# Optimization experiments

Hardware: AMD Instinct MI355X
Metric: run time of the kernel (lower is better)

The kernel has to match this reference:

```python
import jax, jax.numpy as jnp
import numpy as np

EPS = 1e-8


def _dtw_distance(cost):
    """Classic DTW DP: D[i,j] = cost[i,j] + min(D[i-1,j], D[i-1,j-1], D[i,j-1]).
    Rows are processed with lax.scan; the within-row left-to-right recurrence
    D[j] = min(a[j], D[j-1] + c[j]) is solved in closed form as a min-plus scan:
    with S = cumsum(c), D = cummin(a - S) + S.
    """
    # first row: only horizontal moves -> running cumsum
    d0 = jnp.cumsum(cost[0])

    def row_step(prev, c):
        # prev: D[i-1, :]  (shape [m]);  c: cost[i, :]
        prev_diag = jnp.concatenate([jnp.full((1,), jnp.inf, prev.dtype), prev[:-1]])
        a = c + jnp.minimum(prev, prev_diag)          # candidate from above / diagonal
        S = jnp.cumsum(c)
        d = jax.lax.cummin(a - S) + S                 # folds in the left-neighbor path
        return d, None

    d_last, _ = jax.lax.scan(row_step, d0, cost[1:])
    return d_last[-1]


def setup_inputs() -> dict:
    key = jax.random.key(0)
    k1, k2 = jax.random.split(key)
    N1, N2, D = 4096, 4096, 1024
    return {
        "trajectory1": jax.random.normal(k1, (N1, D), dtype=jnp.float32),
        "trajectory2": jax.random.normal(k2, (N2, D), dtype=jnp.float32),
    }


def reference(trajectory1, trajectory2):
    # cosine distance matrix: 1 - <t1_hat, t2_hat>
    t1 = trajectory1 / (jnp.linalg.norm(trajectory1, axis=-1, keepdims=True) + EPS)
    t2 = trajectory2 / (jnp.linalg.norm(trajectory2, axis=-1, keepdims=True) + EPS)
    cost = 1.0 - jnp.einsum('id,jd->ij', t1, t2)      # [N1, N2]
    distance = _dtw_distance(cost)
    similarity = 1.0 / (1.0 + distance)
    return similarity
```

## Files before the change

kernel.cpp:

```cpp
#include <hip/hip_runtime.h>
#include <hip/hip_bf16.h>
#include <stdint.h>

#define KDIM 1024
#define NROW 4096
#define NCOL 4096
#define INFV 1e30f
#define INFBITS 0x7149F2CAu
#define BM 128
#define BK 32

#define SKROWS 4160
#define NBLK32 130
#define NWG    16

typedef __bf16 bf16x8 __attribute__((ext_vector_type(8)));
typedef float f32x4 __attribute__((ext_vector_type(4)));

#define CFENCE asm volatile("" ::: "memory")

__device__ __forceinline__ unsigned short f2bf(float f) {
    __hip_bfloat16 h = __float2bfloat16(f);
    return *reinterpret_cast<unsigned short*>(&h);
}

__device__ __forceinline__ void gll16(const void* gsrc, void* ldst) {
    __builtin_amdgcn_global_load_lds(
        (const __attribute__((address_space(1))) void*)gsrc,
        (__attribute__((address_space(3))) void*)ldst, 16, 0, 0);
}

__global__ __launch_bounds__(256) void normalize_bf16(
    const float* __restrict__ t1, const float* __restrict__ t2,
    unsigned short* __restrict__ o1, unsigned short* __restrict__ o2)
{
    int b = blockIdx.x;
    int t = threadIdx.x;
    const float* src;
    unsigned short* dst;
    if (b < NROW) { src = t1 + (size_t)b * KDIM;          dst = o1 + (size_t)b * KDIM; }
    else          { src = t2 + (size_t)(b - NROW) * KDIM; dst = o2 + (size_t)(b - NROW) * KDIM; }

    float4 v = reinterpret_cast<const float4*>(src)[t];
    float ss = v.x * v.x + v.y * v.y + v.z * v.z + v.w * v.w;
    #pragma unroll
    for (int d = 32; d >= 1; d >>= 1) ss += __shfl_xor(ss, d, 64);

    __shared__ float wsum[4];
    int wave = t >> 6;
    if ((t & 63) == 0) wsum[wave] = ss;
    __syncthreads();
    float inv = 1.0f / (sqrtf(wsum[0] + wsum[1] + wsum[2] + wsum[3]) + 1e-8f);

    ushort4 o;
    o.x = f2bf(v.x * inv);
    o.y = f2bf(v.y * inv);
    o.z = f2bf(v.z * inv);
    o.w = f2bf(v.w * inv);
    reinterpret_cast<ushort4*>(dst)[t] = o;
}

__global__ __launch_bounds__(256) void gemm_cost(
    const unsigned short* __restrict__ A,
    const unsigned short* __restrict__ B,
    unsigned short* __restrict__ Cs)
{
    __shared__ __align__(16) unsigned short As[BM * BK];
    __shared__ __align__(16) unsigned short Bs[BM * BK];

    int t    = threadIdx.x;
    int lane = t & 63;
    int wave = t >> 6;
    int i0   = blockIdx.y * BM;
    int j0   = blockIdx.x * BM;

    f32x4 acc[4][4];
    f32x4 zero = {0.f, 0.f, 0.f, 0.f};
    #pragma unroll
    for (int m = 0; m < 4; ++m)
        #pragma unroll
        for (int n = 0; n < 4; ++n) acc[m][n] = zero;

    int frow = lane & 15;
    int fk   = (lane >> 4) * 8;
    int wr   = (wave >> 1) * 64;
    int wc   = (wave & 1) * 64;

    int srow = t >> 2;
    int scb  = (t & 3) * 8;

    uint4 ra0, ra1, rb0, rb1;
    {
        ra0 = *reinterpret_cast<const uint4*>(A + (size_t)(i0 + srow) * KDIM + scb);
        ra1 = *reinterpret_cast<const uint4*>(A + (size_t)(i0 + 64 + srow) * KDIM + scb);
        rb0 = *reinterpret_cast<const uint4*>(B + (size_t)(j0 + srow) * KDIM + scb);
        rb1 = *reinterpret_cast<const uint4*>(B + (size_t)(j0 + 64 + srow) * KDIM + scb);
    }

    for (int k0 = 0; k0 < KDIM; k0 += BK) {
        __syncthreads();
        *reinterpret_cast<uint4*>(As + (size_t)t * 8)         = ra0;
        *reinterpret_cast<uint4*>(As + (size_t)(256 + t) * 8) = ra1;
        *reinterpret_cast<uint4*>(Bs + (size_t)t * 8)         = rb0;
        *reinterpret_cast<uint4*>(Bs + (size_t)(256 + t) * 8) = rb1;
        __syncthreads();

        if (k0 + BK < KDIM) {
            int kn = k0 + BK;
            ra0 = *reinterpret_cast<const uint4*>(A + (size_t)(i0 + srow) * KDIM + kn + scb);
            ra1 = *reinterpret_cast<const uint4*>(A + (size_t)(i0 + 64 + srow) * KDIM + kn + scb);
            rb0 = *reinterpret_cast<const uint4*>(B + (size_t)(j0 + srow) * KDIM + kn + scb);
            rb1 = *reinterpret_cast<const uint4*>(B + (size_t)(j0 + 64 + srow) * KDIM + kn + scb);
        }

        bf16x8 af[4], bfr[4];
        #pragma unroll
        for (int m = 0; m < 4; ++m)
            af[m] = *reinterpret_cast<const bf16x8*>(As + (wr + m * 16 + frow) * BK + fk);
        #pragma unroll
        for (int n = 0; n < 4; ++n)
            bfr[n] = *reinterpret_cast<const bf16x8*>(Bs + (wc + n * 16 + frow) * BK + fk);

        #pragma unroll
        for (int m = 0; m < 4; ++m)
            #pragma unroll
            for (int n = 0; n < 4; ++n)
                acc[m][n] = __builtin_amdgcn_mfma_f32_16x16x32_bf16(af[m], bfr[n], acc[m][n], 0, 0, 0);
    }

    int crow = (lane >> 4) * 4;
    int ccol = lane & 15;
    #pragma unroll
    for (int n = 0; n < 4; ++n) {
        const int j  = j0 + wc + n * 16 + ccol;
        const int Lj = (j >> 2) & 63;
        #pragma unroll
        for (int m = 0; m < 4; ++m) {
            const int ibase = i0 + wr + m * 16 + crow;
            #pragma unroll
            for (int q = 0; q < 4; ++q)
                Cs[(size_t)(ibase + q + Lj) * NCOL + j] = f2bf(1.0f - acc[m][n][q]);
        }
    }
}

__global__ __launch_bounds__(256) void ring_init(unsigned long long* __restrict__ ring)
{
    int i = blockIdx.x * 256 + threadIdx.x;
    ring[(size_t)15 * NROW + i] =
        ((unsigned long long)INFBITS << 32) | (unsigned)(i + 1);
}

__global__ __launch_bounds__(64, 1) void dtw_systolic(
    const unsigned short* __restrict__ cost,
    unsigned long long* __restrict__ ring,
    float* __restrict__ out)
{
    __shared__ __align__(16) unsigned char clds[2 * 16384];
    __shared__ float outT[32];
    __shared__ float outD[64];

    const int w    = blockIdx.x;
    const int lane = threadIdx.x;
    const char* skewb = (const char*)cost;
    const unsigned long long* rseg = ring + (size_t)((w == 0) ? 15 : (w - 1)) * NROW;
    unsigned long long* wseg = (w < NWG - 1) ? (ring + (size_t)w * NROW)
                                             : (ring + (size_t)NWG * NROW + w * 64);
    unsigned long long* garb = ring + (size_t)NWG * NROW + w * 64;
    const unsigned l32 = (unsigned)(lane & 31);
    const unsigned stripeByte = (unsigned)w * 512u + ((unsigned)(lane & 31) << 4);

    float pd0 = INFV, pd1 = INFV, pd2 = INFV, pd3 = INFV;
    float lprev = (w == 0 && lane == 0) ? 0.0f : INFV;
    float d3p = INFV;
    unsigned ansb = INFBITS;
    unsigned long long rv0 = 0, rv1 = 0, rv2 = 0;

#define GLL16S(STG) { int sg_ = (STG); sg_ = sg_ < 0 ? 0 : (sg_ > NBLK32 - 1 ? NBLK32 - 1 : sg_); \
    unsigned char* ldsb_ = clds + (sg_ & 1) * 16384; \
    _Pragma("unroll") \
    for (int g_ = 0; g_ < 16; ++g_) { \
        int sr_ = 32 * sg_ + 2 * g_ + (lane >> 5); \
        if (sr_ > SKROWS - 1) sr_ = SKROWS - 1; \
        gll16(skewb + (size_t)sr_ * 8192 + stripeByte, ldsb_ + g_ * 1024); } }

#define RINGLD(DST, BI) { int pb_ = (BI); pb_ = pb_ < 0 ? 0 : (pb_ > 127 ? 127 : pb_); \
    const unsigned off_ = (32u * (unsigned)pb_ + l32) * 8u; \
    asm volatile("global_load_dwordx2 %0, %1, %2 sc0 sc1" \
                 : "=v"(DST) : "v"(off_), "s"(rseg) : "memory"); }

#define DCOMP(K, CU) { \
    const unsigned rbK = (unsigned)__builtin_amdgcn_readlane(rvhi, (K)); \
    const float lcur = __uint_as_float((unsigned)__builtin_amdgcn_update_dpp( \
        (int)rbK, (int)__float_as_uint(d3p), 0x138, 0xf, 0xf, false)); \
    const float c0 = __uint_as_float(CU.x << 16); \
    const float c1 = __uint_as_float(CU.x & 0xffff0000u); \
    const float c2 = __uint_as_float(CU.y << 16); \
    const float c3 = __uint_as_float(CU.y & 0xffff0000u); \
    const float n0 = c0 + fminf(pd0, lprev); \
    const float n1 = c1 + fminf(pd1, pd0); \
    const float n2 = c2 + fminf(pd2, pd1); \
    const float n3 = c3 + fminf(pd3, pd2); \
    const float e0 = fminf(lcur + c0, n0); \
    const float e1 = fminf(e0 + c1, n1); \
    const float e2 = fminf(e1 + c2, n2); \
    const float e3 = fminf(e2 + c3, n3); \
    float* sp_ = (lane == 63) ? &outT[K] : &outD[lane]; \
    *sp_ = e3; \
    ansb = (tjb + (K) == 4158) ? __float_as_uint(e3) : ansb; \
    lprev = lcur; d3p = e3; \
    pd0 = e0; pd1 = e1; pd2 = e2; pd3 = e3; }

    GLL16S(0)
    RINGLD(rv0, 0) RINGLD(rv1, 1) RINGLD(rv2, 2)
    CFENCE;

    #pragma unroll 1
    for (int ib = 0; ib < NBLK32; ++ib) {
        GLL16S(ib + 1)
        unsigned long long rvN;
        RINGLD(rvN, ib + 3)
        CFENCE;
        asm volatile("s_waitcnt vmcnt(19)" : "+v"(rv0) :: "memory");

        if (ib < 128) {
            const unsigned expt = 32u * (unsigned)ib + l32 + 1u;
            while (__ballot((unsigned)rv0 == expt) != ~0ull)
                rv0 = __hip_atomic_load(rseg + 32u * (unsigned)ib + l32,
                                        __ATOMIC_RELAXED, __HIP_MEMORY_SCOPE_AGENT);
        }
        const int rvhi = (int)(unsigned)(rv0 >> 32);

        const uint2* lu = reinterpret_cast<const uint2*>(
            clds + (ib & 1) * 16384 + (lane << 3));
        const uint2 cc0  = lu[0 * 64],  cc1  = lu[1 * 64];
        const uint2 cc2  = lu[2 * 64],  cc3  = lu[3 * 64];
        const uint2 cc4  = lu[4 * 64],  cc5  = lu[5 * 64];
        const uint2 cc6  = lu[6 * 64],  cc7  = lu[7 * 64];
        const uint2 cc8  = lu[8 * 64],  cc9  = lu[9 * 64];
        const uint2 cc10 = lu[10 * 64], cc11 = lu[11 * 64];
        const uint2 cc12 = lu[12 * 64], cc13 = lu[13 * 64];
        const uint2 cc14 = lu[14 * 64], cc15 = lu[15 * 64];
        const uint2 cc16 = lu[16 * 64], cc17 = lu[17 * 64];
        const uint2 cc18 = lu[18 * 64], cc19 = lu[19 * 64];
        const uint2 cc20 = lu[20 * 64], cc21 = lu[21 * 64];
        const uint2 cc22 = lu[22 * 64], cc23 = lu[23 * 64];
        const uint2 cc24 = lu[24 * 64], cc25 = lu[25 * 64];
        const uint2 cc26 = lu[26 * 64], cc27 = lu[27 * 64];
        const uint2 cc28 = lu[28 * 64], cc29 = lu[29 * 64];
        const uint2 cc30 = lu[30 * 64], cc31 = lu[31 * 64];

        const int rowbase = 32 * ib - 63;
        const int tjb = 32 * ib;

        DCOMP(0,  cc0)  DCOMP(1,  cc1)  DCOMP(2,  cc2)  DCOMP(3,  cc3)
        DCOMP(4,  cc4)  DCOMP(5,  cc5)  DCOMP(6,  cc6)  DCOMP(7,  cc7)
        DCOMP(8,  cc8)  DCOMP(9,  cc9)  DCOMP(10, cc10) DCOMP(11, cc11)
        DCOMP(12, cc12) DCOMP(13, cc13) DCOMP(14, cc14) DCOMP(15, cc15)
        DCOMP(16, cc16) DCOMP(17, cc17) DCOMP(18, cc18) DCOMP(19, cc19)
        DCOMP(20, cc20) DCOMP(21, cc21) DCOMP(22, cc22) DCOMP(23, cc23)
        DCOMP(24, cc24) DCOMP(25, cc25) DCOMP(26, cc26) DCOMP(27, cc27)
        DCOMP(28, cc28) DCOMP(29, cc29) DCOMP(30, cc30) DCOMP(31, cc31)

        {
            const float bv = outT[l32];
            const int r = rowbase + (int)l32;
            const bool valid = (lane < 32) && (r >= 0) && (r <= 4095) &&
                               (w < NWG - 1);
            if (lane < 32) {
                const unsigned long long pk =
                    ((unsigned long long)__float_as_uint(bv) << 32) | (unsigned)(r + 1);
                unsigned long long* sp = valid ? (wseg + r) : (garb + lane);
                (void)__hip_atomic_exchange(sp, pk, __ATOMIC_RELAXED,
                                            __HIP_MEMORY_SCOPE_AGENT);
            }
        }
        CFENCE;

        rv0 = rv1; rv1 = rv2; rv2 = rvN;
    }

#undef GLL16S
#undef RINGLD
#undef DCOMP

    if (w == NWG - 1 && lane == 63) out[0] = 1.0f / (1.0f + __uint_as_float(ansb));
}

extern "C" void kernel_launch(void* const* d_in, const int* in_sizes, int n_in,
                              void* d_out, int out_size, void* d_ws, size_t ws_size,
                              hipStream_t stream)
{
    const float* t1 = (const float*)d_in[0];
    const float* t2 = (const float*)d_in[1];
    float* out = (float*)d_out;

    char* ws = (char*)d_ws;
    unsigned short* t1n  = (unsigned short*)ws;
    unsigned short* t2n  = (unsigned short*)(ws + (size_t)NROW * KDIM * 2);
    unsigned short* skew = (unsigned short*)(ws + (size_t)16 * 1024 * 1024);
    unsigned long long* ring = (unsigned long long*)(ws + (size_t)52 * 1024 * 1024);

    hipMemsetAsync(ring, 0, (size_t)15 * NROW * 8, stream);
    ring_init<<<NROW / 256, 256, 0, stream>>>(ring);
    normalize_bf16<<<2 * NROW, 256, 0, stream>>>(t1, t2, t1n, t2n);
    gemm_cost<<<dim3(NCOL / BM, NROW / BM), 256, 0, stream>>>(t1n, t2n, skew);
    dtw_systolic<<<NWG, 64, 0, stream>>>(skew, ring, out);
}
```

Baseline: 517.0 us.

## Process two 32-column blocks per iteration in DTW systolic wavefront loop

```diff
diff --git a/kernel.cpp b/kernel.cpp
--- a/kernel.cpp
+++ b/kernel.cpp
@@ -12,6 +12,7 @@
 
 #define SKROWS 4160
 #define NBLK32 130
+#define NPAIR  65
 #define NWG    16
 
 typedef __bf16 bf16x8 __attribute__((ext_vector_type(8)));
@@ -156,41 +157,39 @@
     unsigned long long* __restrict__ ring,
     float* __restrict__ out)
 {
-    __shared__ __align__(16) unsigned char clds[2 * 16384];
-    __shared__ float outT[32];
+    __shared__ __align__(16) unsigned char clds[4 * 16384];
+    __shared__ float outT[128];
     __shared__ float outD[64];
 
     const int w    = blockIdx.x;
     const int lane = threadIdx.x;
     const char* skewb = (const char*)cost;
     const unsigned long long* rseg = ring + (size_t)((w == 0) ? 15 : (w - 1)) * NROW;
-    unsigned long long* wseg = (w < NWG - 1) ? (ring + (size_t)w * NROW)
-                                             : (ring + (size_t)NWG * NROW + w * 64);
+    unsigned long long* wseg = ring + (size_t)w * NROW;
     unsigned long long* garb = ring + (size_t)NWG * NROW + w * 64;
-    const unsigned l32 = (unsigned)(lane & 31);
     const unsigned stripeByte = (unsigned)w * 512u + ((unsigned)(lane & 31) << 4);
 
     float pd0 = INFV, pd1 = INFV, pd2 = INFV, pd3 = INFV;
     float lprev = (w == 0 && lane == 0) ? 0.0f : INFV;
     float d3p = INFV;
     unsigned ansb = INFBITS;
-    unsigned long long rv0 = 0, rv1 = 0, rv2 = 0;
-
-#define GLL16S(STG) { int sg_ = (STG); sg_ = sg_ < 0 ? 0 : (sg_ > NBLK32 - 1 ? NBLK32 - 1 : sg_); \
-    unsigned char* ldsb_ = clds + (sg_ & 1) * 16384; \
+    unsigned long long rv0 = 0;
+
+#define GLL16S(STG) { const int stg_ = (STG); \
+    unsigned char* ldsb_ = clds + (stg_ & 3) * 16384; \
     _Pragma("unroll") \
     for (int g_ = 0; g_ < 16; ++g_) { \
-        int sr_ = 32 * sg_ + 2 * g_ + (lane >> 5); \
+        int sr_ = 32 * stg_ + 2 * g_ + (lane >> 5); \
         if (sr_ > SKROWS - 1) sr_ = SKROWS - 1; \
         gll16(skewb + (size_t)sr_ * 8192 + stripeByte, ldsb_ + g_ * 1024); } }
 
-#define RINGLD(DST, BI) { int pb_ = (BI); pb_ = pb_ < 0 ? 0 : (pb_ > 127 ? 127 : pb_); \
-    const unsigned off_ = (32u * (unsigned)pb_ + l32) * 8u; \
+#define RINGLD(DST, PG) { int pg_ = (PG); pg_ = pg_ < 0 ? 0 : (pg_ > 63 ? 63 : pg_); \
+    const unsigned off_ = (64u * (unsigned)pg_ + (unsigned)lane) * 8u; \
     asm volatile("global_load_dwordx2 %0, %1, %2 sc0 sc1" \
                  : "=v"(DST) : "v"(off_), "s"(rseg) : "memory"); }
 
-#define DCOMP(K, CU) { \
-    const unsigned rbK = (unsigned)__builtin_amdgcn_readlane(rvhi, (K)); \
+#define DCOMP(K, CU, RL) { \
+    const unsigned rbK = (unsigned)__builtin_amdgcn_readlane(rvhi, (RL)); \
     const float lcur = __uint_as_float((unsigned)__builtin_amdgcn_update_dpp( \
         (int)rbK, (int)__float_as_uint(d3p), 0x138, 0xf, 0xf, false)); \
     const float c0 = __uint_as_float(CU.x << 16); \
@@ -205,84 +204,92 @@
     const float e1 = fminf(e0 + c1, n1); \
     const float e2 = fminf(e1 + c2, n2); \
     const float e3 = fminf(e2 + c3, n3); \
-    float* sp_ = (lane == 63) ? &outT[K] : &outD[lane]; \
+    float* sp_ = (lane == 63) ? &outT[(unsigned)(rowbase + (K)) & 127u] \
+                              : &outD[lane]; \
     *sp_ = e3; \
     ansb = (tjb + (K) == 4158) ? __float_as_uint(e3) : ansb; \
     lprev = lcur; d3p = e3; \
     pd0 = e0; pd1 = e1; pd2 = e2; pd3 = e3; }
 
-    GLL16S(0)
-    RINGLD(rv0, 0) RINGLD(rv1, 1) RINGLD(rv2, 2)
+#define BLOCK32(SLOT, RB, TJ, RLOFF) { \
+    const uint2* lu = reinterpret_cast<const uint2*>( \
+        clds + (SLOT) * 16384 + (lane << 3)); \
+    const int rowbase = (RB); const int tjb = (TJ); \
+    const uint2 cc0  = lu[0 * 64],  cc1  = lu[1 * 64]; \
+    const uint2 cc2  = lu[2 * 64],  cc3  = lu[3 * 64]; \
+    const uint2 cc4  = lu[4 * 64],  cc5  = lu[5 * 64]; \
+    const uint2 cc6  = lu[6 * 64],  cc7  = lu[7 * 64]; \
+    const uint2 cc8  = lu[8 * 64],  cc9  = lu[9 * 64]; \
+    const uint2 cc10 = lu[10 * 64], cc11 = lu[11 * 64]; \
+    const uint2 cc12 = lu[12 * 64], cc13 = lu[13 * 64]; \
+    const uint2 cc14 = lu[14 * 64], cc15 = lu[15 * 64]; \
+    const uint2 cc16 = lu[16 * 64], cc17 = lu[17 * 64]; \
+    const uint2 cc18 = lu[18 * 64], cc19 = lu[19 * 64]; \
+    const uint2 cc20 = lu[20 * 64], cc21 = lu[21 * 64]; \
+    const uint2 cc22 = lu[22 * 64], cc23 = lu[23 * 64]; \
+    const uint2 cc24 = lu[24 * 64], cc25 = lu[25 * 64]; \
+    const uint2 cc26 = lu[26 * 64], cc27 = lu[27 * 64]; \
+    const uint2 cc28 = lu[28 * 64], cc29 = lu[29 * 64]; \
+    const uint2 cc30 = lu[30 * 64], cc31 = lu[31 * 64]; \
+    DCOMP(0,  cc0,  (RLOFF)+0)  DCOMP(1,  cc1,  (RLOFF)+1) \
+    DCOMP(2,  cc2,  (RLOFF)+2)  DCOMP(3,  cc3,  (RLOFF)+3) \
+    DCOMP(4,  cc4,  (RLOFF)+4)  DCOMP(5,  cc5,  (RLOFF)+5) \
+    DCOMP(6,  cc6,  (RLOFF)+6)  DCOMP(7,  cc7,  (RLOFF)+7) \
+    DCOMP(8,  cc8,  (RLOFF)+8)  DCOMP(9,  cc9,  (RLOFF)+9) \
+    DCOMP(10, cc10, (RLOFF)+10) DCOMP(11, cc11, (RLOFF)+11) \
+    DCOMP(12, cc12, (RLOFF)+12) DCOMP(13, cc13, (RLOFF)+13) \
+    DCOMP(14, cc14, (RLOFF)+14) DCOMP(15, cc15, (RLOFF)+15) \
+    DCOMP(16, cc16, (RLOFF)+16) DCOMP(17, cc17, (RLOFF)+17) \
+    DCOMP(18, cc18, (RLOFF)+18) DCOMP(19, cc19, (RLOFF)+19) \
+    DCOMP(20, cc20, (RLOFF)+20) DCOMP(21, cc21, (RLOFF)+21) \
+    DCOMP(22, cc22, (RLOFF)+22) DCOMP(23, cc23, (RLOFF)+23) \
+    DCOMP(24, cc24, (RLOFF)+24) DCOMP(25, cc25, (RLOFF)+25) \
+    DCOMP(26, cc26, (RLOFF)+26) DCOMP(27, cc27, (RLOFF)+27) \
+    DCOMP(28, cc28, (RLOFF)+28) DCOMP(29, cc29, (RLOFF)+29) \
+    DCOMP(30, cc30, (RLOFF)+30) DCOMP(31, cc31, (RLOFF)+31) }
+
+    GLL16S(0) GLL16S(1)
+    RINGLD(rv0, 0)
+    __hip_atomic_store(garb + lane, 0ull, __ATOMIC_RELAXED, __HIP_MEMORY_SCOPE_AGENT);
     CFENCE;
 
     #pragma unroll 1
-    for (int ib = 0; ib < NBLK32; ++ib) {
-        GLL16S(ib + 1)
+    for (int m = 0; m < NPAIR; ++m) {
+        GLL16S(2 * m + 2) GLL16S(2 * m + 3)
         unsigned long long rvN;
-        RINGLD(rvN, ib + 3)
+        RINGLD(rvN, m + 1)
         CFENCE;
-        asm volatile("s_waitcnt vmcnt(19)" : "+v"(rv0) :: "memory");
-
-        if (ib < 128) {
-            const unsigned expt = 32u * (unsigned)ib + l32 + 1u;
+        asm volatile("s_waitcnt vmcnt(34)" : "+v"(rv0) :: "memory");
+
+        if (m < 64) {
+            const unsigned expt = 64u * (unsigned)m + (unsigned)lane + 1u;
             while (__ballot((unsigned)rv0 == expt) != ~0ull)
-                rv0 = __hip_atomic_load(rseg + 32u * (unsigned)ib + l32,
+                rv0 = __hip_atomic_load(rseg + 64u * (unsigned)m + (unsigned)lane,
                                         __ATOMIC_RELAXED, __HIP_MEMORY_SCOPE_AGENT);
         }
         const int rvhi = (int)(unsigned)(rv0 >> 32);
 
-        const uint2* lu = reinterpret_cast<const uint2*>(
-            clds + (ib & 1) * 16384 + (lane << 3));
-        const uint2 cc0  = lu[0 * 64],  cc1  = lu[1 * 64];
-        const uint2 cc2  = lu[2 * 64],  cc3  = lu[3 * 64];
-        const uint2 cc4  = lu[4 * 64],  cc5  = lu[5 * 64];
-        const uint2 cc6  = lu[6 * 64],  cc7  = lu[7 * 64];
-        const uint2 cc8  = lu[8 * 64],  cc9  = lu[9 * 64];
-        const uint2 cc10 = lu[10 * 64], cc11 = lu[11 * 64];
-        const uint2 cc12 = lu[12 * 64], cc13 = lu[13 * 64];
-        const uint2 cc14 = lu[14 * 64], cc15 = lu[15 * 64];
-        const uint2 cc16 = lu[16 * 64], cc17 = lu[17 * 64];
-        const uint2 cc18 = lu[18 * 64], cc19 = lu[19 * 64];
-        const uint2 cc20 = lu[20 * 64], cc21 = lu[21 * 64];
-        const uint2 cc22 = lu[22 * 64], cc23 = lu[23 * 64];
-        const uint2 cc24 = lu[24 * 64], cc25 = lu[25 * 64];
-        const uint2 cc26 = lu[26 * 64], cc27 = lu[27 * 64];
-        const uint2 cc28 = lu[28 * 64], cc29 = lu[29 * 64];
-        const uint2 cc30 = lu[30 * 64], cc31 = lu[31 * 64];
-
-        const int rowbase = 32 * ib - 63;
-        const int tjb = 32 * ib;
-
-        DCOMP(0,  cc0)  DCOMP(1,  cc1)  DCOMP(2,  cc2)  DCOMP(3,  cc3)
-        DCOMP(4,  cc4)  DCOMP(5,  cc5)  DCOMP(6,  cc6)  DCOMP(7,  cc7)
-        DCOMP(8,  cc8)  DCOMP(9,  cc9)  DCOMP(10, cc10) DCOMP(11, cc11)
-        DCOMP(12, cc12) DCOMP(13, cc13) DCOMP(14, cc14) DCOMP(15, cc15)
-        DCOMP(16, cc16) DCOMP(17, cc17) DCOMP(18, cc18) DCOMP(19, cc19)
-        DCOMP(20, cc20) DCOMP(21, cc21) DCOMP(22, cc22) DCOMP(23, cc23)
-        DCOMP(24, cc24) DCOMP(25, cc25) DCOMP(26, cc26) DCOMP(27, cc27)
-        DCOMP(28, cc28) DCOMP(29, cc29) DCOMP(30, cc30) DCOMP(31, cc31)
+        BLOCK32((2 * m) & 3,     64 * m - 63,      64 * m,      0)
+        BLOCK32((2 * m + 1) & 3, 64 * m + 32 - 63, 64 * m + 32, 32)
 
         {
-            const float bv = outT[l32];
-            const int r = rowbase + (int)l32;
-            const bool valid = (lane < 32) && (r >= 0) && (r <= 4095) &&
-                               (w < NWG - 1);
-            if (lane < 32) {
-                const unsigned long long pk =
-                    ((unsigned long long)__float_as_uint(bv) << 32) | (unsigned)(r + 1);
-                unsigned long long* sp = valid ? (wseg + r) : (garb + lane);
-                (void)__hip_atomic_exchange(sp, pk, __ATOMIC_RELAXED,
-                                            __HIP_MEMORY_SCOPE_AGENT);
-            }
+            const int r = 64 * (m - 1) + lane;
+            const float bv = outT[(unsigned)r & 127u];
+            const bool valid = (m >= 1) && (w < NWG - 1);
+            const unsigned long long pk =
+                ((unsigned long long)__float_as_uint(bv) << 32) | (unsigned)(r + 1);
+            unsigned long long* sp = valid ? (wseg + r) : (garb + lane);
+            __hip_atomic_store(sp, pk, __ATOMIC_RELAXED, __HIP_MEMORY_SCOPE_AGENT);
         }
         CFENCE;
 
-        rv0 = rv1; rv1 = rv2; rv2 = rvN;
+        rv0 = rvN;
     }
 
 #undef GLL16S
 #undef RINGLD
 #undef DCOMP
+#undef BLOCK32
 
     if (w == NWG - 1 && lane == 63) out[0] = 1.0f / (1.0f + __uint_as_float(ansb));
 }
```

Measured after the change: 538.5 us. +4.2%, slower.
